# Performance work log

Hardware: AMD Instinct MI355X
Metric: run time of the kernel (lower is better)

The kernel has to match this reference:

```python
import jax, jax.numpy as jnp
import numpy as np

B, T, C = 4, 2048, 1024
H = 16  # NUM_HEADS
HD = C // H  # head_dim = 64


def setup_inputs() -> dict:
    key = jax.random.key(0)
    k1, k2, k3 = jax.random.split(key, 3)
    x = jax.random.normal(k1, (B, T, C), dtype=jnp.float32)
    # nn.Linear weights: stored as [out, in]; apply as x @ W.T
    W_attn = jax.random.normal(k2, (3 * C, C), dtype=jnp.float32) * (1.0 / np.sqrt(C))
    W_proj = jax.random.normal(k3, (C, C), dtype=jnp.float32) * (1.0 / np.sqrt(C))
    return {"x": x, "W_attn": W_attn, "W_proj": W_proj}


def reference(x, W_attn, W_proj):
    Bv, Tv, Cv = x.shape
    qkv = x @ W_attn.T  # [B, T, 3C]
    q, k, v = jnp.split(qkv, 3, axis=2)
    # [B, H, T, HD]
    q = q.reshape(Bv, Tv, H, HD).transpose(0, 2, 1, 3)
    k = k.reshape(Bv, Tv, H, HD).transpose(0, 2, 1, 3)
    v = v.reshape(Bv, Tv, H, HD).transpose(0, 2, 1, 3)
    att = jnp.einsum("bhqd,bhkd->bhqk", q, k) * (1.0 / np.sqrt(HD))
    causal = jnp.tril(jnp.ones((Tv, Tv), dtype=bool))
    att = jnp.where(causal[None, None, :, :], att, -jnp.inf)
    att = jax.nn.softmax(att, axis=-1)
    y = jnp.einsum("bhqk,bhkd->bhqd", att, v)
    y = y.transpose(0, 2, 1, 3).reshape(Bv, Tv, Cv)
    return y @ W_proj.T
```

## Files before the change

kernel.cpp:

```cpp
#include <hip/hip_runtime.h>

typedef _Float16 f16;
typedef _Float16 half8 __attribute__((ext_vector_type(8)));
typedef _Float16 half4v __attribute__((ext_vector_type(4)));
typedef __fp16 fp16x2 __attribute__((ext_vector_type(2)));
typedef float floatx4 __attribute__((ext_vector_type(4)));
typedef unsigned int uint;

constexpr int Bsz = 4, Tseq = 2048, Cdim = 1024, NH = 16, HDim = 64;
constexpr int Mtok = Bsz * Tseq;
constexpr int NQT = Tseq / 64;
constexpr float QSCALE = 0.18033688f;

#define GLDS16(src, dst) __builtin_amdgcn_global_load_lds( \
    (const __attribute__((address_space(1))) void*)(src),  \
    (__attribute__((address_space(3))) void*)(dst), 16, 0, 0)

__device__ __forceinline__ float fexp2(float x) { return __builtin_amdgcn_exp2f(x); }
__device__ __forceinline__ uint pkrtz(float a, float b) {
  fp16x2 h = __builtin_amdgcn_cvt_pkrtz(a, b);
  return __builtin_bit_cast(uint, h);
}

__global__ void cvt3_kernel(const float* __restrict__ x, const float* __restrict__ wa,
                            const float* __restrict__ wp,
                            f16* __restrict__ xh, f16* __restrict__ wah, f16* __restrict__ wph) {
  constexpr int nx = Mtok * Cdim, nwa = 3 * Cdim * Cdim, nwp = Cdim * Cdim;
  int i = (blockIdx.x * blockDim.x + threadIdx.x) * 4;
  const float* src; f16* dst; int off;
  if (i < nx)            { src = x;  dst = xh;  off = i; }
  else if (i < nx + nwa) { src = wa; dst = wah; off = i - nx; }
  else                   { src = wp; dst = wph; off = i - nx - nwa; }
  float4 v = *(const float4*)(src + off);
  half4v o;
  o[0] = (f16)v.x; o[1] = (f16)v.y; o[2] = (f16)v.z; o[3] = (f16)v.w;
  *(half4v*)(dst + off) = o;
}

template<int EPI>
__device__ __forceinline__ void gemm_body(f16* As, f16* Bs,
    const f16* __restrict__ X, const f16* __restrict__ W,
    float* __restrict__ outF,
    f16* __restrict__ q_out, f16* __restrict__ k_out, f16* __restrict__ v_out,
    int N, int K, int bid)
{
  constexpr int BK = 32;
  const int tid = threadIdx.x;
  const int wave = tid >> 6;
  const int lane = tid & 63;
  const int g = lane >> 4, lm = lane & 15;
  const int nbn = N / 128;
  const int bm = bid / nbn;
  const int bn = bid % nbn;
  const int m0 = bm * 128, n0 = bn * 128;
  const int wr = wave >> 1, wc = wave & 1;

  floatx4 acc[4][4];
#pragma unroll
  for (int i = 0; i < 4; ++i)
#pragma unroll
    for (int j = 0; j < 4; ++j) acc[i][j] = (floatx4)0.0f;

  for (int k0 = 0; k0 < K; k0 += BK) {
    __syncthreads();
#pragma unroll
    for (int t = 0; t < 2; ++t) {
      int row = (wave * 2 + t) * 16 + (lane >> 2);
      int cg = (lane & 3) ^ ((row >> 1) & 3);
      const f16* srcA = X + (size_t)(m0 + row) * K + k0 + cg * 8;
      GLDS16(srcA, (char*)As + (wave * 2 + t) * 1024);
      const f16* srcB = W + (size_t)(n0 + row) * K + k0 + cg * 8;
      GLDS16(srcB, (char*)Bs + (wave * 2 + t) * 1024);
    }
    __syncthreads();

    half8 af[4], bf[4];
#pragma unroll
    for (int i = 0; i < 4; ++i) {
      int rowa = wr * 64 + i * 16 + lm;
      int cga = g ^ ((rowa >> 1) & 3);
      af[i] = *(const half8*)((const char*)As + rowa * 64 + cga * 16);
      int rowb = wc * 64 + i * 16 + lm;
      int cgb = g ^ ((rowb >> 1) & 3);
      bf[i] = *(const half8*)((const char*)Bs + rowb * 64 + cgb * 16);
    }
#pragma unroll
    for (int i = 0; i < 4; ++i)
#pragma unroll
      for (int j = 0; j < 4; ++j)
        acc[i][j] = __builtin_amdgcn_mfma_f32_16x16x32_f16(af[i], bf[j], acc[i][j], 0, 0, 0);
  }

#pragma unroll
  for (int i = 0; i < 4; ++i) {
#pragma unroll
    for (int j = 0; j < 4; ++j) {
#pragma unroll
      for (int r = 0; r < 4; ++r) {
        int m = m0 + wr * 64 + i * 16 + 4 * g + r;
        int n = n0 + wc * 64 + j * 16 + lm;
        float v = acc[i][j][r];
        if constexpr (EPI == 1) {
          outF[(size_t)m * N + n] = v;
        } else if constexpr (EPI == 0) {
          int which = n >> 10;
          int inner = n & 1023;
          int h = inner >> 6, hd = inner & 63;
          int b = m >> 11, t = m & 2047;
          if (which == 0) {
            v *= QSCALE;
            q_out[(((size_t)(b * NH + h)) * Tseq + t) * HDim + hd] = (f16)v;
          } else {
            k_out[(((size_t)(b * NH + h)) * Tseq + t) * HDim + hd] = (f16)v;
          }
        } else {
          int h = m >> 6, hd = m & 63;
          int b = n >> 11, t = n & 2047;
          v_out[(((size_t)(b * NH + h)) * HDim + hd) * Tseq + t] = (f16)v;
        }
      }
    }
  }
}

__global__ __launch_bounds__(256)
void qkv_kernel(const f16* __restrict__ xh, const f16* __restrict__ wAh,
                f16* __restrict__ Qh, f16* __restrict__ Kh, f16* __restrict__ Vth) {
  __shared__ __align__(16) f16 As[128 * 32];
  __shared__ __align__(16) f16 Bs[128 * 32];
  if (blockIdx.x < 1024)
    gemm_body<0>(As, Bs, xh, wAh, nullptr, Qh, Kh, nullptr, 2048, Cdim, blockIdx.x);
  else
    gemm_body<2>(As, Bs, wAh + (size_t)2048 * Cdim, xh, nullptr, nullptr, nullptr, Vth,
                 Mtok, Cdim, blockIdx.x - 1024);
}

__global__ __launch_bounds__(256)
void proj_kernel(const f16* __restrict__ yh, const f16* __restrict__ wPh, float* __restrict__ out) {
  __shared__ __align__(16) f16 As[128 * 32];
  __shared__ __align__(16) f16 Bs[128 * 32];
  gemm_body<1>(As, Bs, yh, wPh, out, nullptr, nullptr, nullptr, Cdim, Cdim, blockIdx.x);
}

__device__ __forceinline__ void softmax_tile(floatx4* s, float& l_run,
                                             bool diag, int j0, int qg, char* pwrow, int g, int lm) {
  if (diag) {
#pragma unroll
    for (int nf = 0; nf < 4; ++nf)
#pragma unroll
      for (int r = 0; r < 4; ++r)
        if (j0 + nf * 16 + 4 * g + r > qg) s[nf][r] = -1e30f;
  }
  float rs = 0.f;
#pragma unroll
  for (int nf = 0; nf < 4; ++nf) {
    float p0 = fexp2(s[nf][0]), p1 = fexp2(s[nf][1]);
    float p2 = fexp2(s[nf][2]), p3 = fexp2(s[nf][3]);
    rs += (p0 + p1) + (p2 + p3);
    uint lo = pkrtz(p0, p1), hi = pkrtz(p2, p3);
    int slot = 2 * nf + (g >> 1);
    uint2 u; u.x = lo; u.y = hi;
    *(uint2*)(pwrow + 16 * (slot ^ (lm & 7)) + 8 * (g & 1)) = u;
  }
  l_run += rs;
}

__device__ __forceinline__ void store_o(const floatx4* acc, float l, int q0w, int g, int lm,
                                        f16* __restrict__ Y, int b, int h) {
  l += __shfl_xor(l, 16, 64);
  l += __shfl_xor(l, 32, 64);
#pragma unroll
  for (int r = 0; r < 4; ++r) {
    float lq = __shfl(l, 4 * g + r, 64);
    float inv = 1.0f / lq;
    int t = q0w + 4 * g + r;
    size_t base = ((size_t)(b * Tseq + t)) * Cdim + h * HDim;
#pragma unroll
    for (int ng = 0; ng < 4; ++ng)
      Y[base + ng * 16 + lm] = (f16)(acc[ng][r] * inv);
  }
}

__global__ __launch_bounds__(256)
void attn_kernel(const f16* __restrict__ Q, const f16* __restrict__ Kg,
                 const f16* __restrict__ Vt, f16* __restrict__ Y)
{
  __shared__ __align__(16) char smem[40960];
  int wg = blockIdx.x;
  int lin = (wg & 7) * 128 + (wg >> 3);
  const int p  = lin & 15;
  const int bh = lin >> 4;
  const int qtA = p, qtB = NQT - 1 - p;
  const int ntB = NQT - p;
  const f16* Qb  = Q  + (size_t)bh * Tseq * HDim;
  const f16* Kb  = Kg + (size_t)bh * Tseq * HDim;
  const f16* Vtb = Vt + (size_t)bh * HDim * Tseq;

  const int tid = threadIdx.x, w = tid >> 6, lane = tid & 63;
  const int g = lane >> 4, lm = lane & 15;
  char* pwrow = smem + 32768 + w * 2048 + lm * 128;

  const int q0A = qtA * 64, q0B = qtB * 64;
  const int qgA = q0A + w * 16 + lm, qgB = q0B + w * 16 + lm;

  half8 qfA0 = *(const half8*)(Qb + (size_t)(q0A + w * 16 + lm) * HDim + g * 8);
  half8 qfA1 = *(const half8*)(Qb + (size_t)(q0A + w * 16 + lm) * HDim + 32 + g * 8);
  half8 qfB0 = *(const half8*)(Qb + (size_t)(q0B + w * 16 + lm) * HDim + g * 8);
  half8 qfB1 = *(const half8*)(Qb + (size_t)(q0B + w * 16 + lm) * HDim + 32 + g * 8);

  floatx4 accA[4], accB[4];
  float lA = 0.f, lB = 0.f;
#pragma unroll
  for (int ng = 0; ng < 4; ++ng) { accA[ng] = (floatx4)0.f; accB[ng] = (floatx4)0.f; }

  const int srow = w * 8 + (lane >> 3);
  const int sslot = lane & 7;

  auto stage = [&](int j0s, int buf) {
#pragma unroll
    for (int t = 0; t < 2; ++t) {
      int row = srow + t * 32;
      int cg = sslot ^ (row & 7);
      GLDS16(Kb + (size_t)(j0s + row) * HDim + cg * 8,
             smem + buf * 8192 + (w * 8 + t * 32) * 128);
      GLDS16(Vtb + (size_t)row * Tseq + j0s + cg * 8,
             smem + 16384 + buf * 8192 + (w * 8 + t * 32) * 128);
    }
  };

  stage(0, 0);

  for (int jt = 0; jt < ntB; ++jt) {
    const int cur = jt & 1;
    const int j0 = jt * 64;
    const bool activeA = (jt <= p);

    if (jt + 1 < ntB) {
      stage(j0 + 64, cur ^ 1);
      asm volatile("s_waitcnt vmcnt(4)" ::: "memory");
    } else {
      asm volatile("s_waitcnt vmcnt(0)" ::: "memory");
    }
    __builtin_amdgcn_s_barrier();

    char* kb   = smem + cur * 8192;
    char* vbuf = smem + 16384 + cur * 8192;

    floatx4 sA[4], sB[4];
    __builtin_amdgcn_s_setprio(1);
    if (activeA) {
#pragma unroll
      for (int nf = 0; nf < 4; ++nf) {
        half8 kf0 = *(const half8*)(kb + (nf * 16 + lm) * 128 + 16 * ((g)     ^ (lm & 7)));
        half8 kf1 = *(const half8*)(kb + (nf * 16 + lm) * 128 + 16 * ((4 + g) ^ (lm & 7)));
        sB[nf] = __builtin_amdgcn_mfma_f32_16x16x32_f16(kf0, qfB0, (floatx4)0.f, 0, 0, 0);
        sB[nf] = __builtin_amdgcn_mfma_f32_16x16x32_f16(kf1, qfB1, sB[nf], 0, 0, 0);
        sA[nf] = __builtin_amdgcn_mfma_f32_16x16x32_f16(kf0, qfA0, (floatx4)0.f, 0, 0, 0);
        sA[nf] = __builtin_amdgcn_mfma_f32_16x16x32_f16(kf1, qfA1, sA[nf], 0, 0, 0);
      }
    } else {
#pragma unroll
      for (int nf = 0; nf < 4; ++nf) {
        half8 kf0 = *(const half8*)(kb + (nf * 16 + lm) * 128 + 16 * ((g)     ^ (lm & 7)));
        half8 kf1 = *(const half8*)(kb + (nf * 16 + lm) * 128 + 16 * ((4 + g) ^ (lm & 7)));
        sB[nf] = __builtin_amdgcn_mfma_f32_16x16x32_f16(kf0, qfB0, (floatx4)0.f, 0, 0, 0);
        sB[nf] = __builtin_amdgcn_mfma_f32_16x16x32_f16(kf1, qfB1, sB[nf], 0, 0, 0);
      }
    }
    __builtin_amdgcn_s_setprio(0);

    softmax_tile(sB, lB, jt == qtB, j0, qgB, pwrow, g, lm);
    half8 paB0 = *(const half8*)(pwrow + 16 * ((g)     ^ (lm & 7)));
    half8 paB1 = *(const half8*)(pwrow + 16 * ((4 + g) ^ (lm & 7)));
    half8 paA0 = paB0, paA1 = paB1;
    if (activeA) {
      softmax_tile(sA, lA, jt == qtA, j0, qgA, pwrow, g, lm);
      paA0 = *(const half8*)(pwrow + 16 * ((g)     ^ (lm & 7)));
      paA1 = *(const half8*)(pwrow + 16 * ((4 + g) ^ (lm & 7)));
    }

    __builtin_amdgcn_s_setprio(1);
    if (activeA) {
#pragma unroll
      for (int c = 0; c < 2; ++c)
#pragma unroll
        for (int ng = 0; ng < 4; ++ng) {
          half8 vbf = *(const half8*)(vbuf + (ng * 16 + lm) * 128 + 16 * ((4 * c + g) ^ (lm & 7)));
          accB[ng] = __builtin_amdgcn_mfma_f32_16x16x32_f16(c ? paB1 : paB0, vbf, accB[ng], 0, 0, 0);
          accA[ng] = __builtin_amdgcn_mfma_f32_16x16x32_f16(c ? paA1 : paA0, vbf, accA[ng], 0, 0, 0);
        }
    } else {
#pragma unroll
      for (int c = 0; c < 2; ++c)
#pragma unroll
        for (int ng = 0; ng < 4; ++ng) {
          half8 vbf = *(const half8*)(vbuf + (ng * 16 + lm) * 128 + 16 * ((4 * c + g) ^ (lm & 7)));
          accB[ng] = __builtin_amdgcn_mfma_f32_16x16x32_f16(c ? paB1 : paB0, vbf, accB[ng], 0, 0, 0);
        }
    }
    __builtin_amdgcn_s_setprio(0);

    __builtin_amdgcn_s_barrier();
  }

  const int b = bh >> 4, h = bh & 15;
  store_o(accA, lA, q0A + 16 * w, g, lm, Y, b, h);
  store_o(accB, lB, q0B + 16 * w, g, lm, Y, b, h);
}

extern "C" void kernel_launch(void* const* d_in, const int* in_sizes, int n_in,
                              void* d_out, int out_size, void* d_ws, size_t ws_size,
                              hipStream_t stream)
{
  const float* x      = (const float*)d_in[0];
  const float* W_attn = (const float*)d_in[1];
  const float* W_proj = (const float*)d_in[2];
  float* out = (float*)d_out;

  char* ws = (char*)d_ws;
  f16* xh  = (f16*)(ws);
  f16* wAh = (f16*)(ws + (size_t)(16u << 20));
  f16* wPh = (f16*)(ws + (size_t)(22u << 20));
  f16* Qh  = (f16*)(ws + (size_t)(24u << 20));
  f16* Kh  = (f16*)(ws + (size_t)(40u << 20));
  f16* Vth = (f16*)(ws + (size_t)(56u << 20));
  f16* yh  = xh;

  constexpr int ntot = (Mtok * Cdim + 3 * Cdim * Cdim + Cdim * Cdim) / 4;
  cvt3_kernel<<<(ntot + 255) / 256, 256, 0, stream>>>(x, W_attn, W_proj, xh, wAh, wPh);

  qkv_kernel<<<dim3(1536), 256, 0, stream>>>(xh, wAh, Qh, Kh, Vth);

  attn_kernel<<<dim3(1024), 256, 0, stream>>>(Qh, Kh, Vth, yh);

  proj_kernel<<<dim3((Mtok / 128) * (Cdim / 128)), 256, 0, stream>>>(yh, wPh, out);
}
```

Measured before the change: 183.4 us.

## Serialize paired query tiles in attention loop and swizzle GEMM block order

The attention kernel used to process its two paired query tiles (A and B) together, sharing K/V loads for the overlapping prefix. It now runs them one after the other in a single loop of NQT+1 iterations: tile B first, then tile A, reloading Q and resetting the accumulators in between. This cuts register pressure and branch duplication, but the shared K/V prefix is now loaded twice. The QKV and projection GEMMs also remap block IDs with an XCD-style swizzle to improve cache locality across chiplets.

After: 172.3 us. 6.1% less time.

```diff
diff --git a/kernel.cpp b/kernel.cpp
--- a/kernel.cpp
+++ b/kernel.cpp
@@ -128,18 +128,20 @@
                 f16* __restrict__ Qh, f16* __restrict__ Kh, f16* __restrict__ Vth) {
   __shared__ __align__(16) f16 As[128 * 32];
   __shared__ __align__(16) f16 Bs[128 * 32];
-  if (blockIdx.x < 1024)
-    gemm_body<0>(As, Bs, xh, wAh, nullptr, Qh, Kh, nullptr, 2048, Cdim, blockIdx.x);
+  int sbid = (blockIdx.x & 7) * 192 + (blockIdx.x >> 3);
+  if (sbid < 1024)
+    gemm_body<0>(As, Bs, xh, wAh, nullptr, Qh, Kh, nullptr, 2048, Cdim, sbid);
   else
     gemm_body<2>(As, Bs, wAh + (size_t)2048 * Cdim, xh, nullptr, nullptr, nullptr, Vth,
-                 Mtok, Cdim, blockIdx.x - 1024);
+                 Mtok, Cdim, sbid - 1024);
 }
 
 __global__ __launch_bounds__(256)
 void proj_kernel(const f16* __restrict__ yh, const f16* __restrict__ wPh, float* __restrict__ out) {
   __shared__ __align__(16) f16 As[128 * 32];
   __shared__ __align__(16) f16 Bs[128 * 32];
-  gemm_body<1>(As, Bs, yh, wPh, out, nullptr, nullptr, nullptr, Cdim, Cdim, blockIdx.x);
+  int sbid = (blockIdx.x & 7) * 64 + (blockIdx.x >> 3);
+  gemm_body<1>(As, Bs, yh, wPh, out, nullptr, nullptr, nullptr, Cdim, Cdim, sbid);
 }
 
 __device__ __forceinline__ void softmax_tile(floatx4* s, float& l_run,
@@ -190,8 +192,7 @@
   int lin = (wg & 7) * 128 + (wg >> 3);
   const int p  = lin & 15;
   const int bh = lin >> 4;
-  const int qtA = p, qtB = NQT - 1 - p;
-  const int ntB = NQT - p;
+  const int itB = NQT - p;
   const f16* Qb  = Q  + (size_t)bh * Tseq * HDim;
   const f16* Kb  = Kg + (size_t)bh * Tseq * HDim;
   const f16* Vtb = Vt + (size_t)bh * HDim * Tseq;
@@ -199,19 +200,17 @@
   const int tid = threadIdx.x, w = tid >> 6, lane = tid & 63;
   const int g = lane >> 4, lm = lane & 15;
   char* pwrow = smem + 32768 + w * 2048 + lm * 128;
-
-  const int q0A = qtA * 64, q0B = qtB * 64;
-  const int qgA = q0A + w * 16 + lm, qgB = q0B + w * 16 + lm;
-
-  half8 qfA0 = *(const half8*)(Qb + (size_t)(q0A + w * 16 + lm) * HDim + g * 8);
-  half8 qfA1 = *(const half8*)(Qb + (size_t)(q0A + w * 16 + lm) * HDim + 32 + g * 8);
-  half8 qfB0 = *(const half8*)(Qb + (size_t)(q0B + w * 16 + lm) * HDim + g * 8);
-  half8 qfB1 = *(const half8*)(Qb + (size_t)(q0B + w * 16 + lm) * HDim + 32 + g * 8);
-
-  floatx4 accA[4], accB[4];
-  float lA = 0.f, lB = 0.f;
-#pragma unroll
-  for (int ng = 0; ng < 4; ++ng) { accA[ng] = (floatx4)0.f; accB[ng] = (floatx4)0.f; }
+  const int b = bh >> 4, h = bh & 15;
+
+  int q0 = (NQT - 1 - p) * 64;
+  int qg = q0 + w * 16 + lm;
+  half8 qf0 = *(const half8*)(Qb + (size_t)(q0 + w * 16 + lm) * HDim + g * 8);
+  half8 qf1 = *(const half8*)(Qb + (size_t)(q0 + w * 16 + lm) * HDim + 32 + g * 8);
+
+  floatx4 acc[4];
+  float l = 0.f;
+#pragma unroll
+  for (int ng = 0; ng < 4; ++ng) acc[ng] = (floatx4)0.f;
 
   const int srow = w * 8 + (lane >> 3);
   const int sslot = lane & 7;
@@ -230,82 +229,65 @@
 
   stage(0, 0);
 
-  for (int jt = 0; jt < ntB; ++jt) {
-    const int cur = jt & 1;
+  for (int it = 0; it < NQT + 1; ++it) {
+    const bool lastB = (it == itB - 1);
+    const bool last  = (it == NQT);
+    const int jt = (it < itB) ? it : it - itB;
     const int j0 = jt * 64;
-    const bool activeA = (jt <= p);
-
-    if (jt + 1 < ntB) {
-      stage(j0 + 64, cur ^ 1);
+
+    if (!last) {
+      const int itn = it + 1;
+      const int jtn = (itn < itB) ? itn : itn - itB;
+      stage(jtn * 64, itn & 1);
       asm volatile("s_waitcnt vmcnt(4)" ::: "memory");
     } else {
       asm volatile("s_waitcnt vmcnt(0)" ::: "memory");
     }
     __builtin_amdgcn_s_barrier();
 
-    char* kb   = smem + cur * 8192;
-    char* vbuf = smem + 16384 + cur * 8192;
-
-    floatx4 sA[4], sB[4];
+    char* kb   = smem + (it & 1) * 8192;
+    char* vbuf = smem + 16384 + (it & 1) * 8192;
+
+    floatx4 s[4];
     __builtin_amdgcn_s_setprio(1);
-    if (activeA) {
-#pragma unroll
-      for (int nf = 0; nf < 4; ++nf) {
-        half8 kf0 = *(const half8*)(kb + (nf * 16 + lm) * 128 + 16 * ((g)     ^ (lm & 7)));
-        half8 kf1 = *(const half8*)(kb + (nf * 16 + lm) * 128 + 16 * ((4 + g) ^ (lm & 7)));
-        sB[nf] = __builtin_amdgcn_mfma_f32_16x16x32_f16(kf0, qfB0, (floatx4)0.f, 0, 0, 0);
-        sB[nf] = __builtin_amdgcn_mfma_f32_16x16x32_f16(kf1, qfB1, sB[nf], 0, 0, 0);
-        sA[nf] = __builtin_amdgcn_mfma_f32_16x16x32_f16(kf0, qfA0, (floatx4)0.f, 0, 0, 0);
-        sA[nf] = __builtin_amdgcn_mfma_f32_16x16x32_f16(kf1, qfA1, sA[nf], 0, 0, 0);
+#pragma unroll
+    for (int nf = 0; nf < 4; ++nf) {
+      half8 kf0 = *(const half8*)(kb + (nf * 16 + lm) * 128 + 16 * ((g)     ^ (lm & 7)));
+      half8 kf1 = *(const half8*)(kb + (nf * 16 + lm) * 128 + 16 * ((4 + g) ^ (lm & 7)));
+      s[nf] = __builtin_amdgcn_mfma_f32_16x16x32_f16(kf0, qf0, (floatx4)0.f, 0, 0, 0);
+      s[nf] = __builtin_amdgcn_mfma_f32_16x16x32_f16(kf1, qf1, s[nf], 0, 0, 0);
+    }
+    __builtin_amdgcn_s_setprio(0);
+
+    softmax_tile(s, l, lastB || last, j0, qg, pwrow, g, lm);
+    half8 pa0 = *(const half8*)(pwrow + 16 * ((g)     ^ (lm & 7)));
+    half8 pa1 = *(const half8*)(pwrow + 16 * ((4 + g) ^ (lm & 7)));
+
+    __builtin_amdgcn_s_setprio(1);
+#pragma unroll
+    for (int c = 0; c < 2; ++c)
+#pragma unroll
+      for (int ng = 0; ng < 4; ++ng) {
+        half8 vbf = *(const half8*)(vbuf + (ng * 16 + lm) * 128 + 16 * ((4 * c + g) ^ (lm & 7)));
+        acc[ng] = __builtin_amdgcn_mfma_f32_16x16x32_f16(c ? pa1 : pa0, vbf, acc[ng], 0, 0, 0);
       }
-    } else {
-#pragma unroll
-      for (int nf = 0; nf < 4; ++nf) {
-        half8 kf0 = *(const half8*)(kb + (nf * 16 + lm) * 128 + 16 * ((g)     ^ (lm & 7)));
-        half8 kf1 = *(const half8*)(kb + (nf * 16 + lm) * 128 + 16 * ((4 + g) ^ (lm & 7)));
-        sB[nf] = __builtin_amdgcn_mfma_f32_16x16x32_f16(kf0, qfB0, (floatx4)0.f, 0, 0, 0);
-        sB[nf] = __builtin_amdgcn_mfma_f32_16x16x32_f16(kf1, qfB1, sB[nf], 0, 0, 0);
-      }
-    }
     __builtin_amdgcn_s_setprio(0);
 
-    softmax_tile(sB, lB, jt == qtB, j0, qgB, pwrow, g, lm);
-    half8 paB0 = *(const half8*)(pwrow + 16 * ((g)     ^ (lm & 7)));
-    half8 paB1 = *(const half8*)(pwrow + 16 * ((4 + g) ^ (lm & 7)));
-    half8 paA0 = paB0, paA1 = paB1;
-    if (activeA) {
-      softmax_tile(sA, lA, jt == qtA, j0, qgA, pwrow, g, lm);
-      paA0 = *(const half8*)(pwrow + 16 * ((g)     ^ (lm & 7)));
-      paA1 = *(const half8*)(pwrow + 16 * ((4 + g) ^ (lm & 7)));
-    }
-
-    __builtin_amdgcn_s_setprio(1);
-    if (activeA) {
-#pragma unroll
-      for (int c = 0; c < 2; ++c)
-#pragma unroll
-        for (int ng = 0; ng < 4; ++ng) {
-          half8 vbf = *(const half8*)(vbuf + (ng * 16 + lm) * 128 + 16 * ((4 * c + g) ^ (lm & 7)));
-          accB[ng] = __builtin_amdgcn_mfma_f32_16x16x32_f16(c ? paB1 : paB0, vbf, accB[ng], 0, 0, 0);
-          accA[ng] = __builtin_amdgcn_mfma_f32_16x16x32_f16(c ? paA1 : paA0, vbf, accA[ng], 0, 0, 0);
-        }
-    } else {
-#pragma unroll
-      for (int c = 0; c < 2; ++c)
-#pragma unroll
-        for (int ng = 0; ng < 4; ++ng) {
-          half8 vbf = *(const half8*)(vbuf + (ng * 16 + lm) * 128 + 16 * ((4 * c + g) ^ (lm & 7)));
-          accB[ng] = __builtin_amdgcn_mfma_f32_16x16x32_f16(c ? paB1 : paB0, vbf, accB[ng], 0, 0, 0);
-        }
-    }
-    __builtin_amdgcn_s_setprio(0);
-
     __builtin_amdgcn_s_barrier();
-  }
-
-  const int b = bh >> 4, h = bh & 15;
-  store_o(accA, lA, q0A + 16 * w, g, lm, Y, b, h);
-  store_o(accB, lB, q0B + 16 * w, g, lm, Y, b, h);
+
+    if (lastB) {
+      store_o(acc, l, q0 + 16 * w, g, lm, Y, b, h);
+      q0 = p * 64;
+      qg = q0 + w * 16 + lm;
+      qf0 = *(const half8*)(Qb + (size_t)(q0 + w * 16 + lm) * HDim + g * 8);
+      qf1 = *(const half8*)(Qb + (size_t)(q0 + w * 16 + lm) * HDim + 32 + g * 8);
+      l = 0.f;
+#pragma unroll
+      for (int ng = 0; ng < 4; ++ng) acc[ng] = (floatx4)0.f;
+    }
+  }
+
+  store_o(acc, l, q0 + 16 * w, g, lm, Y, b, h);
 }
 
 extern "C" void kernel_launch(void* const* d_in, const int* in_sizes, int n_in,
@@ -333,5 +315,5 @@
 
   attn_kernel<<<dim3(1024), 256, 0, stream>>>(Qh, Kh, Vth, yh);
 
-  proj_kernel<<<dim3((Mtok / 128) * (Cdim / 128)), 256, 0, stream>>>(yh, wPh, out);
-}
+  proj_kernel<<<dim3(512), 256, 0, stream>>>(yh, wPh, out);
+}
```
